# Performance work log

Hardware: AMD Instinct MI355X
Metric: run time of the kernel (lower is better)

The kernel has to match this reference:

```python
import jax, jax.numpy as jnp
import numpy as np
from jax import lax

SIGMA = 1.0
LW = int(4 * SIGMA + 0.5)  # 4 -> 9-tap kernel, matches scipy _gaussian_kernel1d
_xk = np.arange(-LW, LW + 1)
_phi = np.exp(-0.5 * _xk ** 2 / SIGMA ** 2)
GAUSS_K = (_phi / _phi.sum())[::-1].copy()
EPS = 1e-9
HIGH_T, LOW_T = 0.2, 0.1
H = W = 32


def _corr_w(x, k, mode, p):
    # x: (B,H,W); cross-correlate along last dim with 'same' output (torch Conv1d semantics)
    xp = jnp.pad(x, ((0, 0), (0, 0), (p, p)), mode=mode)
    B, Hh, L = xp.shape
    y = lax.conv_general_dilated(xp.reshape(B * Hh, 1, L), k.reshape(1, 1, -1).astype(x.dtype), (1,), 'VALID')
    return y.reshape(B, Hh, L - k.shape[0] + 1)


def _corr_h(x, k, mode, p):
    return jnp.swapaxes(_corr_w(jnp.swapaxes(x, 1, 2), k, mode, p), 1, 2)


def _gauss(x, k):
    # separable gaussian, zero padding (Conv1d padding=lw), both axes
    return _corr_w(_corr_h(x, k, 'constant', LW), k, 'constant', LW)


def _shift(m, di, dj):
    # out[i,j] = m[i+di, j+dj], zeros outside (only interior points are ever selected)
    p = jnp.pad(m, ((0, 0), (1, 1), (1, 1)))
    return p[:, 1 + di:1 + di + H, 1 + dj:1 + dj + W]


def _canny_core(x, mask, with_hyst=True):
    x = x * 0.5 + 0.5
    gray = x[:, 0] * 0.299 + x[:, 1] * 0.587 + x[:, 2] * 0.114  # (B,H,W)
    gk = jnp.asarray(GAUSS_K, gray.dtype)
    bleed = _gauss(mask[:, 0], gk)                      # (1,H,W)
    sm = _gauss(gray, gk) / (bleed + 1e-12)
    s_major = jnp.asarray([-1.0, 0.0, 1.0], sm.dtype)
    s_minor = jnp.asarray([1.0, 2.0, 1.0], sm.dtype)
    # jsobel: derivative along W then smooth along H; isobel: derivative along H then smooth along W
    jsob = _corr_h(_corr_w(sm, s_major, 'edge', 1), s_minor, 'edge', 1)
    isob = _corr_w(_corr_h(sm, s_major, 'edge', 1), s_minor, 'edge', 1)
    ai, aj = jnp.abs(isob), jnp.abs(jsob)
    mag2 = isob ** 2 + jsob ** 2
    mag = jnp.sqrt(mag2 + EPS)
    # binary_erosion of mask with full 3x3 structure, border_value=0
    mb = lax.stop_gradient(mask[0, 0]) != 0
    pm = jnp.pad(mb, 1)
    er2d = jnp.ones((H, W), bool)
    for di in (-1, 0, 1):
        for dj in (-1, 0, 1):
            er2d = er2d & pm[1 + di:1 + di + H, 1 + dj:1 + dj + W]
    # note: torch code builds eroded_mask from batch element 0 only, then reuses for all
    er = (er2d & (lax.stop_gradient(mag2[0]) > 0))[None]  # (1,H,W)
    same = ((isob >= 0) & (jsob >= 0)) | ((isob <= 0) & (jsob <= 0))
    opp = ((isob <= 0) & (jsob >= 0)) | ((isob >= 0) & (jsob <= 0))
    ai_safe = jnp.where(ai > 0, ai, jnp.asarray(1.0, ai.dtype))
    aj_safe = jnp.where(aj > 0, aj, jnp.asarray(1.0, aj.dtype))
    # (selector, w, c1_plus_shift, c2_plus_shift, c1_minus_shift, c2_minus_shift)
    octants = [
        (same & (ai >= aj), aj / (ai + EPS), (1, 0), (1, 1), (-1, 0), (-1, -1)),
        (same & (ai <= aj), ai / aj_safe, (0, 1), (1, 1), (0, -1), (-1, -1)),
        (opp & (ai <= aj), ai / aj_safe, (0, 1), (-1, 1), (0, -1), (1, -1)),
        (opp & (ai >= aj), aj / ai_safe, (-1, 0), (-1, 1), (1, 0), (1, -1)),
    ]
    lm = jnp.zeros(mag.shape, bool)
    for sel, w, p1, p2, m1, m2 in octants:
        pts = er & sel
        ip = _shift(mag, *p2) * w + _shift(mag, *p1) * (1 - w)
        im = _shift(mag, *m2) * w + _shift(mag, *m1) * (1 - w)
        lm = jnp.where(pts, (ip <= mag) & (im <= mag), lm)  # later octants overwrite, like torch
    if not with_hyst:
        return mag, None
    high = lm & (mag >= HIGH_T)
    low = lm & (mag >= LOW_T)

    def dilate(m):
        p = jnp.pad(m, ((0, 0), (1, 1), (1, 1)))
        out = jnp.zeros_like(m)
        for di in (-1, 0, 1):
            for dj in (-1, 0, 1):
                out = out | p[:, 1 + di:1 + di + H, 1 + dj:1 + dj + W]
        return out

    # hysteresis = 8-connected components of `low` that contain a `high` pixel
    def body(c):
        cur, _ = c
        return dilate(cur) & low, cur

    def cond(c):
        cur, prev = c
        return jnp.any(cur != prev)

    final, _ = lax.while_loop(cond, body, (high, jnp.zeros_like(high)))
    return mag, final


def setup_inputs() -> dict:
    key = jax.random.key(0)
    k1, _ = jax.random.split(key)
    x = jax.random.normal(k1, (8192, 3, 32, 32), dtype=jnp.float32)
    mask = jnp.ones((1, 1, 32, 32), dtype=jnp.float32)
    return {"x": x, "mask": mask}


def reference(x, mask):
    mag, final = _canny_core(x, mask, with_hyst=True)
    mf = final.astype(mag.dtype)
    out = mf + mag - lax.stop_gradient(mag)  # straight-through: value==mf, grad flows via mag
    out = (out - 0.5) / 0.5
    return out[:, None]  # (B,1,32,32)
```

## Files before the change

### kernel.cpp

```cpp
#include <hip/hip_runtime.h>
#include <math.h>

#pragma clang fp contract(off)

#define NPIX 1024

__device__ __forceinline__ void compute_gk(float gk[9]) {
    double phi[9];
    #pragma unroll
    for (int t = 0; t < 9; ++t) {
        double d = (double)(t - 4);
        phi[t] = exp(-0.5 * d * d);
    }
    double s = (((phi[0] + phi[1]) + (phi[2] + phi[3])) +
                ((phi[4] + phi[5]) + (phi[6] + phi[7]))) + phi[8];
    #pragma unroll
    for (int t = 0; t < 9; ++t) gk[t] = (float)(phi[t] / s);
}

__device__ __forceinline__ float ldz(const float* b, int i, int j) {
    return (i >= 0 && i < 32 && j >= 0 && j < 32) ? b[(i << 5) + j] : 0.0f;
}
__device__ __forceinline__ float ldc(const float* b, int i, int j) {
    i = i < 0 ? 0 : (i > 31 ? 31 : i);
    j = j < 0 ? 0 : (j > 31 ? 31 : j);
    return b[(i << 5) + j];
}

__device__ __forceinline__ bool nms2(const float* mag, int i, int j, float m, float w,
                                     int p2i, int p2j, int p1i, int p1j,
                                     int m2i, int m2j, int m1i, int m1j) {
    float omw = 1.0f - w;
    float ip = ldz(mag, i + p2i, j + p2j) * w + ldz(mag, i + p1i, j + p1j) * omw;
    float im = ldz(mag, i + m2i, j + m2j) * w + ldz(mag, i + m1i, j + m1j) * omw;
    return (ip <= m) && (im <= m);
}

__global__ __launch_bounds__(256) void canny_pre(const float* __restrict__ x,
                                                 const float* __restrict__ mask,
                                                 float* __restrict__ ws_bleed,
                                                 unsigned int* __restrict__ ws_er,
                                                 float* __restrict__ ws_gk) {
    __shared__ float A[NPIX], Bf[NPIX], C[NPIX], D[NPIX], BL[NPIX];
    __shared__ unsigned int er32[32];
    const int tid = threadIdx.x;
    float gk[9];
    compute_gk(gk);
    if (tid < 9) ws_gk[tid] = gk[tid];

    #pragma unroll
    for (int k = 0; k < 4; ++k) { int p = tid + (k << 8); A[p] = mask[p]; }
    if (tid < 32) er32[tid] = 0u;
    __syncthreads();

    #pragma unroll
    for (int k = 0; k < 4; ++k) {
        int p = tid + (k << 8), i = p >> 5, j = p & 31;
        float s = 0.0f;
        #pragma unroll
        for (int t = 0; t < 9; ++t) s = __fmaf_rn(gk[t], ldz(A, i + t - 4, j), s);
        Bf[p] = s;
    }
    __syncthreads();
    #pragma unroll
    for (int k = 0; k < 4; ++k) {
        int p = tid + (k << 8), i = p >> 5, j = p & 31;
        float s = 0.0f;
        #pragma unroll
        for (int t = 0; t < 9; ++t) s = __fmaf_rn(gk[t], ldz(Bf, i, j + t - 4), s);
        BL[p] = s;
        ws_bleed[p] = s + 1e-12f;
    }

    bool er2d[4];
    #pragma unroll
    for (int k = 0; k < 4; ++k) {
        int p = tid + (k << 8), i = p >> 5, j = p & 31;
        bool e = true;
        for (int di = -1; di <= 1; ++di)
            for (int dj = -1; dj <= 1; ++dj) {
                int ii = i + di, jj = j + dj;
                e = e && (ii >= 0 && ii < 32 && jj >= 0 && jj < 32) && (A[(ii << 5) + jj] != 0.0f);
            }
        er2d[k] = e;
    }
    __syncthreads();

    #pragma unroll
    for (int k = 0; k < 4; ++k) {
        int p = tid + (k << 8);
        float r = x[p]            * 0.5f + 0.5f;
        float g = x[p + NPIX]     * 0.5f + 0.5f;
        float b = x[p + 2 * NPIX] * 0.5f + 0.5f;
        A[p] = r * 0.299f + g * 0.587f + b * 0.114f;
    }
    __syncthreads();
    #pragma unroll
    for (int k = 0; k < 4; ++k) {
        int p = tid + (k << 8), i = p >> 5, j = p & 31;
        float s = 0.0f;
        #pragma unroll
        for (int t = 0; t < 9; ++t) s = __fmaf_rn(gk[t], ldz(A, i + t - 4, j), s);
        Bf[p] = s;
    }
    __syncthreads();
    #pragma unroll
    for (int k = 0; k < 4; ++k) {
        int p = tid + (k << 8), i = p >> 5, j = p & 31;
        float s = 0.0f;
        #pragma unroll
        for (int t = 0; t < 9; ++t) s = __fmaf_rn(gk[t], ldz(Bf, i, j + t - 4), s);
        A[p] = s;
    }
    __syncthreads();
    #pragma unroll
    for (int k = 0; k < 4; ++k) { int p = tid + (k << 8); A[p] = A[p] / (BL[p] + 1e-12f); }
    __syncthreads();
    #pragma unroll
    for (int k = 0; k < 4; ++k) { int p = tid + (k << 8), i = p >> 5, j = p & 31;
        Bf[p] = ldc(A, i, j + 1) - ldc(A, i, j - 1); }
    __syncthreads();
    #pragma unroll
    for (int k = 0; k < 4; ++k) { int p = tid + (k << 8), i = p >> 5, j = p & 31;
        C[p] = (ldc(Bf, i - 1, j) + 2.0f * ldc(Bf, i, j)) + ldc(Bf, i + 1, j); }
    __syncthreads();
    #pragma unroll
    for (int k = 0; k < 4; ++k) { int p = tid + (k << 8), i = p >> 5, j = p & 31;
        Bf[p] = ldc(A, i + 1, j) - ldc(A, i - 1, j); }
    __syncthreads();
    #pragma unroll
    for (int k = 0; k < 4; ++k) { int p = tid + (k << 8), i = p >> 5, j = p & 31;
        D[p] = (ldc(Bf, i, j - 1) + 2.0f * ldc(Bf, i, j)) + ldc(Bf, i, j + 1); }
    __syncthreads();
    #pragma unroll
    for (int k = 0; k < 4; ++k) {
        int p = tid + (k << 8), i = p >> 5, j = p & 31;
        if (er2d[k]) {
            float m2 = D[p] * D[p] + C[p] * C[p];
            if (m2 > 0.0f) atomicOr(&er32[i], 1u << j);
        }
    }
    __syncthreads();
    if (tid < 32) ws_er[tid] = er32[tid];
}

__global__ __launch_bounds__(256) void canny_main(const float* __restrict__ x,
                                                  const float* __restrict__ ws_bleed,
                                                  const unsigned int* __restrict__ ws_er,
                                                  const float* __restrict__ ws_gk,
                                                  float* __restrict__ out) {
    __shared__ float APAD[40 * 32];
    __shared__ float BPAD[32 * 40];
    __shared__ float MPAD[34 * 34];
    __shared__ unsigned int er[32], hi32[32], lo32[32], fin32[32];
    const int tid = threadIdx.x;
    const int b = blockIdx.x;

    float gk[9];
    #pragma unroll
    for (int t = 0; t < 9; ++t) gk[t] = ws_gk[t];

    APAD[tid < 128 ? tid : 1024 + tid] = 0.0f;
    { int r = tid >> 3, c8 = tid & 7; BPAD[r * 40 + c8 + (c8 < 4 ? 0 : 32)] = 0.0f; }
    #pragma unroll
    for (int t = 0; t < 5; ++t) { int idx = tid + (t << 8); if (idx < 34 * 34) MPAD[idx] = 0.0f; }
    if (tid < 32) er[tid] = ws_er[tid];

    {
        const float4* xr = (const float4*)(x + (size_t)b * 3 * NPIX);
        float4 r4 = xr[tid];
        float4 g4 = xr[tid + 256];
        float4 b4 = xr[tid + 512];
        int p = tid << 2, i = p >> 5, j = p & 31;
        float4 gy;
        gy.x = (r4.x * 0.5f + 0.5f) * 0.299f + (g4.x * 0.5f + 0.5f) * 0.587f + (b4.x * 0.5f + 0.5f) * 0.114f;
        gy.y = (r4.y * 0.5f + 0.5f) * 0.299f + (g4.y * 0.5f + 0.5f) * 0.587f + (b4.y * 0.5f + 0.5f) * 0.114f;
        gy.z = (r4.z * 0.5f + 0.5f) * 0.299f + (g4.z * 0.5f + 0.5f) * 0.587f + (b4.z * 0.5f + 0.5f) * 0.114f;
        gy.w = (r4.w * 0.5f + 0.5f) * 0.299f + (g4.w * 0.5f + 0.5f) * 0.587f + (b4.w * 0.5f + 0.5f) * 0.114f;
        *(float4*)&APAD[((i + 4) << 5) + j] = gy;
    }
    __syncthreads();

    #pragma unroll
    for (int k = 0; k < 4; ++k) {
        int p = tid + (k << 8), i = p >> 5, j = p & 31;
        float s = 0.0f;
        #pragma unroll
        for (int t = 0; t < 9; ++t) s = __fmaf_rn(gk[t], APAD[((i + t) << 5) + j], s);
        BPAD[i * 40 + j + 4] = s;
    }
    __syncthreads();

    #pragma unroll
    for (int k = 0; k < 4; ++k) {
        int p = tid + (k << 8), i = p >> 5, j = p & 31;
        float s = 0.0f;
        #pragma unroll
        for (int t = 0; t < 9; ++t) s = __fmaf_rn(gk[t], BPAD[i * 40 + j + t], s);
        APAD[((i + 4) << 5) + j] = s / ws_bleed[p];
    }
    __syncthreads();

    float jsr[4], isr[4], mr[4];
    const float* S = &APAD[4 << 5];
    #pragma unroll
    for (int k = 0; k < 4; ++k) {
        int p = tid + (k << 8), i = p >> 5, j = p & 31;
        int im1 = i > 0 ? i - 1 : 0, ip1 = i < 31 ? i + 1 : 31;
        int jm1 = j > 0 ? j - 1 : 0, jp1 = j < 31 ? j + 1 : 31;
        float tm = S[(im1 << 5) + jp1] - S[(im1 << 5) + jm1];
        float t0 = S[(i   << 5) + jp1] - S[(i   << 5) + jm1];
        float tp = S[(ip1 << 5) + jp1] - S[(ip1 << 5) + jm1];
        float jsob = (tm + 2.0f * t0) + tp;
        float um = S[(ip1 << 5) + jm1] - S[(im1 << 5) + jm1];
        float u0 = S[(ip1 << 5) + j  ] - S[(im1 << 5) + j  ];
        float up = S[(ip1 << 5) + jp1] - S[(im1 << 5) + jp1];
        float isob = (um + 2.0f * u0) + up;
        jsr[k] = jsob; isr[k] = isob;
        float m = sqrtf((isob * isob + jsob * jsob) + 1e-9f);
        mr[k] = m;
        MPAD[(i + 1) * 34 + (j + 1)] = m;
    }
    __syncthreads();

    #pragma unroll
    for (int k = 0; k < 4; ++k) {
        int p = tid + (k << 8), i = p >> 5, j = p & 31;
        float iv = isr[k], jv = jsr[k], m = mr[k];
        float ai = fabsf(iv), aj = fabsf(jv);
        bool same = (iv >= 0.0f && jv >= 0.0f) || (iv <= 0.0f && jv <= 0.0f);
        bool opp  = (iv <= 0.0f && jv >= 0.0f) || (iv >= 0.0f && jv <= 0.0f);
        bool age  = (ai >= aj), ale = (ai <= aj);
        int oct = (opp && age) ? 3 : (opp && ale) ? 2 : (same && ale) ? 1 : 0;
        float ais = ai > 0.0f ? ai : 1.0f;
        float ajs = aj > 0.0f ? aj : 1.0f;
        float num = (oct == 3 || oct == 0) ? aj : ai;
        float den = (oct == 3) ? ais : (oct == 0) ? (ai + 1e-9f) : ajs;
        float w = num / den;
        float omw = 1.0f - w;
        int p2i = (oct >= 2) ? -1 : 1;
        int p1i = (oct == 0) ? 1 : (oct == 3) ? -1 : 0;
        int p1j = (oct == 1 || oct == 2) ? 1 : 0;
        int base = (i + 1) * 34 + (j + 1);
        float ip = MPAD[base + p2i * 34 + 1] * w + MPAD[base + p1i * 34 + p1j] * omw;
        float im = MPAD[base - p2i * 34 - 1] * w + MPAD[base - p1i * 34 - p1j] * omw;
        bool lm = (ip <= m) && (im <= m);
        bool eb = (er[i] >> j) & 1u;
        unsigned long long bh = __ballot(lm && eb && (m >= 0.2f));
        unsigned long long bl = __ballot(lm && eb && (m >= 0.1f));
        if ((tid & 63) == 0) {
            int r0 = (k << 3) + ((tid >> 6) << 1);
            hi32[r0]     = (unsigned int)bh;
            hi32[r0 + 1] = (unsigned int)(bh >> 32);
            lo32[r0]     = (unsigned int)bl;
            lo32[r0 + 1] = (unsigned int)(bl >> 32);
        }
    }
    __syncthreads();

    if (tid < 64) {
        unsigned int lw  = (tid < 32) ? lo32[tid] : 0u;
        unsigned int cur = (tid < 32) ? hi32[tid] : 0u;
        for (;;) {
            unsigned int sp  = cur | (cur << 1) | (cur >> 1);
            unsigned int upv = (unsigned int)__shfl((int)sp, (tid + 63) & 63, 64);
            if (tid == 0) upv = 0u;
            unsigned int dnv = (unsigned int)__shfl((int)sp, (tid + 1) & 63, 64);
            unsigned int nxt = (sp | upv | dnv) & lw;
            bool ch = (nxt != cur);
            cur = nxt;
            if (__ballot((int)ch) == 0ull) break;
        }
        if (tid < 32) fin32[tid] = cur;
    }
    __syncthreads();

    {
        int p = tid << 2, i = p >> 5, j = p & 31;
        unsigned int row = fin32[i];
        float4 o;
        o.x = ((row >> (j    )) & 1u) ? 1.0f : -1.0f;
        o.y = ((row >> (j + 1)) & 1u) ? 1.0f : -1.0f;
        o.z = ((row >> (j + 2)) & 1u) ? 1.0f : -1.0f;
        o.w = ((row >> (j + 3)) & 1u) ? 1.0f : -1.0f;
        ((float4*)(out + (size_t)b * NPIX))[tid] = o;
    }
}

extern "C" void kernel_launch(void* const* d_in, const int* in_sizes, int n_in,
                              void* d_out, int out_size, void* d_ws, size_t ws_size,
                              hipStream_t stream) {
    const float* x    = (const float*)d_in[0];
    const float* mask = (const float*)d_in[1];
    float* out        = (float*)d_out;
    float* ws_bleed   = (float*)d_ws;
    unsigned int* ws_er = (unsigned int*)(ws_bleed + NPIX);
    float* ws_gk      = (float*)(ws_er + 32);
    int Bn = in_sizes[0] / (3 * NPIX);

    hipLaunchKernelGGL(canny_pre, dim3(1), dim3(256), 0, stream, x, mask, ws_bleed, ws_er, ws_gk);
    hipLaunchKernelGGL(canny_main, dim3(Bn), dim3(256), 0, stream, x, ws_bleed, ws_er, ws_gk, out);
}
```

Measured before the change: 51.65 us.

## Process two images per block with interleaved float2 shared-memory layout

Each block now handles two batch images. Their grayscale and blurred values are interleaved as float2 in shared memory, so each LDS access and gaussian tap loop serves both images. Hysteresis runs on a full 64-lane wave with 32 rows per image, with boundaries masked between the two halves. This halves the number of blocks and spreads the per-block overhead (barriers, padding zeroing, loading er/gk) over two images. In exchange it raises shared memory and register use per block, which may reduce occupancy, and the hysteresis loop now runs until the slower of the two images converges.

```diff
diff --git a/kernel.cpp b/kernel.cpp
--- a/kernel.cpp
+++ b/kernel.cpp
@@ -25,15 +25,6 @@
     i = i < 0 ? 0 : (i > 31 ? 31 : i);
     j = j < 0 ? 0 : (j > 31 ? 31 : j);
     return b[(i << 5) + j];
-}
-
-__device__ __forceinline__ bool nms2(const float* mag, int i, int j, float m, float w,
-                                     int p2i, int p2j, int p1i, int p1j,
-                                     int m2i, int m2j, int m1i, int m1j) {
-    float omw = 1.0f - w;
-    float ip = ldz(mag, i + p2i, j + p2j) * w + ldz(mag, i + p1i, j + p1j) * omw;
-    float im = ldz(mag, i + m2i, j + m2j) * w + ldz(mag, i + m1i, j + m1j) * omw;
-    return (ip <= m) && (im <= m);
 }
 
 __global__ __launch_bounds__(256) void canny_pre(const float* __restrict__ x,
@@ -144,49 +135,61 @@
     if (tid < 32) ws_er[tid] = er32[tid];
 }
 
-__global__ __launch_bounds__(256) void canny_main(const float* __restrict__ x,
-                                                  const float* __restrict__ ws_bleed,
-                                                  const unsigned int* __restrict__ ws_er,
-                                                  const float* __restrict__ ws_gk,
-                                                  float* __restrict__ out) {
-    __shared__ float APAD[40 * 32];
-    __shared__ float BPAD[32 * 40];
-    __shared__ float MPAD[34 * 34];
-    __shared__ unsigned int er[32], hi32[32], lo32[32], fin32[32];
+__global__ __launch_bounds__(256) void canny_main2(const float* __restrict__ x,
+                                                   const float* __restrict__ ws_bleed,
+                                                   const unsigned int* __restrict__ ws_er,
+                                                   const float* __restrict__ ws_gk,
+                                                   float* __restrict__ out, int Bn) {
+    __shared__ float2 APAD[40 * 32];
+    __shared__ float2 BPAD[32 * 40];
+    __shared__ float  MP[2][34 * 34];
+    __shared__ unsigned int er[32], hi[64], lo[64], fin[64];
     const int tid = threadIdx.x;
-    const int b = blockIdx.x;
+    const int b0 = blockIdx.x * 2;
+    const int b1 = (b0 + 1 < Bn) ? b0 + 1 : b0;
 
     float gk[9];
     #pragma unroll
     for (int t = 0; t < 9; ++t) gk[t] = ws_gk[t];
 
-    APAD[tid < 128 ? tid : 1024 + tid] = 0.0f;
-    { int r = tid >> 3, c8 = tid & 7; BPAD[r * 40 + c8 + (c8 < 4 ? 0 : 32)] = 0.0f; }
-    #pragma unroll
-    for (int t = 0; t < 5; ++t) { int idx = tid + (t << 8); if (idx < 34 * 34) MPAD[idx] = 0.0f; }
+    const float2 z2 = make_float2(0.0f, 0.0f);
+    APAD[tid < 128 ? tid : 1024 + tid] = z2;
+    { int r = tid >> 3, c8 = tid & 7; BPAD[r * 40 + c8 + (c8 < 4 ? 0 : 32)] = z2; }
+    {
+        float* MZ = &MP[0][0];
+        #pragma unroll
+        for (int t = 0; t < 10; ++t) { int idx = tid + (t << 8); if (idx < 2 * 34 * 34) MZ[idx] = 0.0f; }
+    }
     if (tid < 32) er[tid] = ws_er[tid];
 
     {
-        const float4* xr = (const float4*)(x + (size_t)b * 3 * NPIX);
-        float4 r4 = xr[tid];
-        float4 g4 = xr[tid + 256];
-        float4 b4 = xr[tid + 512];
+        const float4* x0 = (const float4*)(x + (size_t)b0 * 3 * NPIX);
+        const float4* x1 = (const float4*)(x + (size_t)b1 * 3 * NPIX);
+        float4 r0 = x0[tid], g0 = x0[tid + 256], c0 = x0[tid + 512];
+        float4 r1 = x1[tid], g1 = x1[tid + 256], c1 = x1[tid + 512];
         int p = tid << 2, i = p >> 5, j = p & 31;
-        float4 gy;
-        gy.x = (r4.x * 0.5f + 0.5f) * 0.299f + (g4.x * 0.5f + 0.5f) * 0.587f + (b4.x * 0.5f + 0.5f) * 0.114f;
-        gy.y = (r4.y * 0.5f + 0.5f) * 0.299f + (g4.y * 0.5f + 0.5f) * 0.587f + (b4.y * 0.5f + 0.5f) * 0.114f;
-        gy.z = (r4.z * 0.5f + 0.5f) * 0.299f + (g4.z * 0.5f + 0.5f) * 0.587f + (b4.z * 0.5f + 0.5f) * 0.114f;
-        gy.w = (r4.w * 0.5f + 0.5f) * 0.299f + (g4.w * 0.5f + 0.5f) * 0.587f + (b4.w * 0.5f + 0.5f) * 0.114f;
-        *(float4*)&APAD[((i + 4) << 5) + j] = gy;
-    }
-    __syncthreads();
-
-    #pragma unroll
-    for (int k = 0; k < 4; ++k) {
-        int p = tid + (k << 8), i = p >> 5, j = p & 31;
-        float s = 0.0f;
-        #pragma unroll
-        for (int t = 0; t < 9; ++t) s = __fmaf_rn(gk[t], APAD[((i + t) << 5) + j], s);
+        float2* dst = &APAD[((i + 4) << 5) + j];
+        dst[0] = make_float2((r0.x * 0.5f + 0.5f) * 0.299f + (g0.x * 0.5f + 0.5f) * 0.587f + (c0.x * 0.5f + 0.5f) * 0.114f,
+                             (r1.x * 0.5f + 0.5f) * 0.299f + (g1.x * 0.5f + 0.5f) * 0.587f + (c1.x * 0.5f + 0.5f) * 0.114f);
+        dst[1] = make_float2((r0.y * 0.5f + 0.5f) * 0.299f + (g0.y * 0.5f + 0.5f) * 0.587f + (c0.y * 0.5f + 0.5f) * 0.114f,
+                             (r1.y * 0.5f + 0.5f) * 0.299f + (g1.y * 0.5f + 0.5f) * 0.587f + (c1.y * 0.5f + 0.5f) * 0.114f);
+        dst[2] = make_float2((r0.z * 0.5f + 0.5f) * 0.299f + (g0.z * 0.5f + 0.5f) * 0.587f + (c0.z * 0.5f + 0.5f) * 0.114f,
+                             (r1.z * 0.5f + 0.5f) * 0.299f + (g1.z * 0.5f + 0.5f) * 0.587f + (c1.z * 0.5f + 0.5f) * 0.114f);
+        dst[3] = make_float2((r0.w * 0.5f + 0.5f) * 0.299f + (g0.w * 0.5f + 0.5f) * 0.587f + (c0.w * 0.5f + 0.5f) * 0.114f,
+                             (r1.w * 0.5f + 0.5f) * 0.299f + (g1.w * 0.5f + 0.5f) * 0.587f + (c1.w * 0.5f + 0.5f) * 0.114f);
+    }
+    __syncthreads();
+
+    #pragma unroll
+    for (int k = 0; k < 4; ++k) {
+        int p = tid + (k << 8), i = p >> 5, j = p & 31;
+        float2 s = z2;
+        #pragma unroll
+        for (int t = 0; t < 9; ++t) {
+            float2 v = APAD[((i + t) << 5) + j];
+            s.x = __fmaf_rn(gk[t], v.x, s.x);
+            s.y = __fmaf_rn(gk[t], v.y, s.y);
+        }
         BPAD[i * 40 + j + 4] = s;
     }
     __syncthreads();
@@ -194,96 +197,132 @@
     #pragma unroll
     for (int k = 0; k < 4; ++k) {
         int p = tid + (k << 8), i = p >> 5, j = p & 31;
-        float s = 0.0f;
-        #pragma unroll
-        for (int t = 0; t < 9; ++t) s = __fmaf_rn(gk[t], BPAD[i * 40 + j + t], s);
-        APAD[((i + 4) << 5) + j] = s / ws_bleed[p];
-    }
-    __syncthreads();
-
-    float jsr[4], isr[4], mr[4];
-    const float* S = &APAD[4 << 5];
+        float2 s = z2;
+        #pragma unroll
+        for (int t = 0; t < 9; ++t) {
+            float2 v = BPAD[i * 40 + j + t];
+            s.x = __fmaf_rn(gk[t], v.x, s.x);
+            s.y = __fmaf_rn(gk[t], v.y, s.y);
+        }
+        float bl = ws_bleed[p];
+        APAD[((i + 4) << 5) + j] = make_float2(s.x / bl, s.y / bl);
+    }
+    __syncthreads();
+
+    float2 jsr[4], isr[4], mr[4];
+    const float2* S = &APAD[4 << 5];
     #pragma unroll
     for (int k = 0; k < 4; ++k) {
         int p = tid + (k << 8), i = p >> 5, j = p & 31;
         int im1 = i > 0 ? i - 1 : 0, ip1 = i < 31 ? i + 1 : 31;
         int jm1 = j > 0 ? j - 1 : 0, jp1 = j < 31 ? j + 1 : 31;
-        float tm = S[(im1 << 5) + jp1] - S[(im1 << 5) + jm1];
-        float t0 = S[(i   << 5) + jp1] - S[(i   << 5) + jm1];
-        float tp = S[(ip1 << 5) + jp1] - S[(ip1 << 5) + jm1];
-        float jsob = (tm + 2.0f * t0) + tp;
-        float um = S[(ip1 << 5) + jm1] - S[(im1 << 5) + jm1];
-        float u0 = S[(ip1 << 5) + j  ] - S[(im1 << 5) + j  ];
-        float up = S[(ip1 << 5) + jp1] - S[(im1 << 5) + jp1];
-        float isob = (um + 2.0f * u0) + up;
-        jsr[k] = jsob; isr[k] = isob;
-        float m = sqrtf((isob * isob + jsob * jsob) + 1e-9f);
-        mr[k] = m;
-        MPAD[(i + 1) * 34 + (j + 1)] = m;
-    }
-    __syncthreads();
-
-    #pragma unroll
-    for (int k = 0; k < 4; ++k) {
-        int p = tid + (k << 8), i = p >> 5, j = p & 31;
-        float iv = isr[k], jv = jsr[k], m = mr[k];
-        float ai = fabsf(iv), aj = fabsf(jv);
-        bool same = (iv >= 0.0f && jv >= 0.0f) || (iv <= 0.0f && jv <= 0.0f);
-        bool opp  = (iv <= 0.0f && jv >= 0.0f) || (iv >= 0.0f && jv <= 0.0f);
-        bool age  = (ai >= aj), ale = (ai <= aj);
-        int oct = (opp && age) ? 3 : (opp && ale) ? 2 : (same && ale) ? 1 : 0;
-        float ais = ai > 0.0f ? ai : 1.0f;
-        float ajs = aj > 0.0f ? aj : 1.0f;
-        float num = (oct == 3 || oct == 0) ? aj : ai;
-        float den = (oct == 3) ? ais : (oct == 0) ? (ai + 1e-9f) : ajs;
-        float w = num / den;
-        float omw = 1.0f - w;
-        int p2i = (oct >= 2) ? -1 : 1;
-        int p1i = (oct == 0) ? 1 : (oct == 3) ? -1 : 0;
-        int p1j = (oct == 1 || oct == 2) ? 1 : 0;
+        float2 smm = S[(im1 << 5) + jm1], sm0 = S[(im1 << 5) + j], smp = S[(im1 << 5) + jp1];
+        float2 s0m = S[(i   << 5) + jm1],                        s0p = S[(i   << 5) + jp1];
+        float2 spm = S[(ip1 << 5) + jm1], sp0 = S[(ip1 << 5) + j], spp = S[(ip1 << 5) + jp1];
+        float2 jsob, isob, m;
+        {
+            float tm = smp.x - smm.x, t0 = s0p.x - s0m.x, tp = spp.x - spm.x;
+            jsob.x = (tm + 2.0f * t0) + tp;
+            float um = spm.x - smm.x, u0 = sp0.x - sm0.x, up = spp.x - smp.x;
+            isob.x = (um + 2.0f * u0) + up;
+            m.x = sqrtf((isob.x * isob.x + jsob.x * jsob.x) + 1e-9f);
+        }
+        {
+            float tm = smp.y - smm.y, t0 = s0p.y - s0m.y, tp = spp.y - spm.y;
+            jsob.y = (tm + 2.0f * t0) + tp;
+            float um = spm.y - smm.y, u0 = sp0.y - sm0.y, up = spp.y - smp.y;
+            isob.y = (um + 2.0f * u0) + up;
+            m.y = sqrtf((isob.y * isob.y + jsob.y * jsob.y) + 1e-9f);
+        }
+        jsr[k] = jsob; isr[k] = isob; mr[k] = m;
+        int mi = (i + 1) * 34 + (j + 1);
+        MP[0][mi] = m.x;
+        MP[1][mi] = m.y;
+    }
+    __syncthreads();
+
+    #pragma unroll
+    for (int k = 0; k < 4; ++k) {
+        int p = tid + (k << 8), i = p >> 5, j = p & 31;
         int base = (i + 1) * 34 + (j + 1);
-        float ip = MPAD[base + p2i * 34 + 1] * w + MPAD[base + p1i * 34 + p1j] * omw;
-        float im = MPAD[base - p2i * 34 - 1] * w + MPAD[base - p1i * 34 - p1j] * omw;
-        bool lm = (ip <= m) && (im <= m);
         bool eb = (er[i] >> j) & 1u;
-        unsigned long long bh = __ballot(lm && eb && (m >= 0.2f));
-        unsigned long long bl = __ballot(lm && eb && (m >= 0.1f));
+        bool hq[2], lq[2];
+        #pragma unroll
+        for (int c = 0; c < 2; ++c) {
+            float iv = c ? isr[k].y : isr[k].x;
+            float jv = c ? jsr[k].y : jsr[k].x;
+            float m  = c ? mr[k].y  : mr[k].x;
+            float ai = fabsf(iv), aj = fabsf(jv);
+            bool same = (iv >= 0.0f && jv >= 0.0f) || (iv <= 0.0f && jv <= 0.0f);
+            bool opp  = (iv <= 0.0f && jv >= 0.0f) || (iv >= 0.0f && jv <= 0.0f);
+            bool age  = (ai >= aj), ale = (ai <= aj);
+            int oct = (opp && age) ? 3 : (opp && ale) ? 2 : (same && ale) ? 1 : 0;
+            float ais = ai > 0.0f ? ai : 1.0f;
+            float ajs = aj > 0.0f ? aj : 1.0f;
+            float num = (oct == 3 || oct == 0) ? aj : ai;
+            float den = (oct == 3) ? ais : (oct == 0) ? (ai + 1e-9f) : ajs;
+            float w = num / den;
+            float omw = 1.0f - w;
+            int p2i = (oct >= 2) ? -1 : 1;
+            int p1i = (oct == 0) ? 1 : (oct == 3) ? -1 : 0;
+            int p1j = (oct == 1 || oct == 2) ? 1 : 0;
+            const float* MC = MP[c];
+            float ip = MC[base + p2i * 34 + 1] * w + MC[base + p1i * 34 + p1j] * omw;
+            float im = MC[base - p2i * 34 - 1] * w + MC[base - p1i * 34 - p1j] * omw;
+            bool lm = (ip <= m) && (im <= m) && eb;
+            hq[c] = lm && (m >= 0.2f);
+            lq[c] = lm && (m >= 0.1f);
+        }
+        unsigned long long bh0 = __ballot(hq[0]);
+        unsigned long long bl0 = __ballot(lq[0]);
+        unsigned long long bh1 = __ballot(hq[1]);
+        unsigned long long bl1 = __ballot(lq[1]);
         if ((tid & 63) == 0) {
             int r0 = (k << 3) + ((tid >> 6) << 1);
-            hi32[r0]     = (unsigned int)bh;
-            hi32[r0 + 1] = (unsigned int)(bh >> 32);
-            lo32[r0]     = (unsigned int)bl;
-            lo32[r0 + 1] = (unsigned int)(bl >> 32);
+            hi[r0]          = (unsigned int)bh0;
+            hi[r0 + 1]      = (unsigned int)(bh0 >> 32);
+            lo[r0]          = (unsigned int)bl0;
+            lo[r0 + 1]      = (unsigned int)(bl0 >> 32);
+            hi[32 + r0]     = (unsigned int)bh1;
+            hi[32 + r0 + 1] = (unsigned int)(bh1 >> 32);
+            lo[32 + r0]     = (unsigned int)bl1;
+            lo[32 + r0 + 1] = (unsigned int)(bl1 >> 32);
         }
     }
     __syncthreads();
 
     if (tid < 64) {
-        unsigned int lw  = (tid < 32) ? lo32[tid] : 0u;
-        unsigned int cur = (tid < 32) ? hi32[tid] : 0u;
+        unsigned int lw  = lo[tid];
+        unsigned int cur = hi[tid];
         for (;;) {
             unsigned int sp  = cur | (cur << 1) | (cur >> 1);
             unsigned int upv = (unsigned int)__shfl((int)sp, (tid + 63) & 63, 64);
-            if (tid == 0) upv = 0u;
+            if ((tid & 31) == 0) upv = 0u;
             unsigned int dnv = (unsigned int)__shfl((int)sp, (tid + 1) & 63, 64);
+            if ((tid & 31) == 31) dnv = 0u;
             unsigned int nxt = (sp | upv | dnv) & lw;
             bool ch = (nxt != cur);
             cur = nxt;
             if (__ballot((int)ch) == 0ull) break;
         }
-        if (tid < 32) fin32[tid] = cur;
+        fin[tid] = cur;
     }
     __syncthreads();
 
     {
         int p = tid << 2, i = p >> 5, j = p & 31;
-        unsigned int row = fin32[i];
-        float4 o;
-        o.x = ((row >> (j    )) & 1u) ? 1.0f : -1.0f;
-        o.y = ((row >> (j + 1)) & 1u) ? 1.0f : -1.0f;
-        o.z = ((row >> (j + 2)) & 1u) ? 1.0f : -1.0f;
-        o.w = ((row >> (j + 3)) & 1u) ? 1.0f : -1.0f;
-        ((float4*)(out + (size_t)b * NPIX))[tid] = o;
+        unsigned int r0w = fin[i], r1w = fin[32 + i];
+        float4 o0, o1;
+        o0.x = ((r0w >> (j    )) & 1u) ? 1.0f : -1.0f;
+        o0.y = ((r0w >> (j + 1)) & 1u) ? 1.0f : -1.0f;
+        o0.z = ((r0w >> (j + 2)) & 1u) ? 1.0f : -1.0f;
+        o0.w = ((r0w >> (j + 3)) & 1u) ? 1.0f : -1.0f;
+        o1.x = ((r1w >> (j    )) & 1u) ? 1.0f : -1.0f;
+        o1.y = ((r1w >> (j + 1)) & 1u) ? 1.0f : -1.0f;
+        o1.z = ((r1w >> (j + 2)) & 1u) ? 1.0f : -1.0f;
+        o1.w = ((r1w >> (j + 3)) & 1u) ? 1.0f : -1.0f;
+        ((float4*)(out + (size_t)b0 * NPIX))[tid] = o0;
+        if (b1 != b0) ((float4*)(out + (size_t)b1 * NPIX))[tid] = o1;
     }
 }
 
@@ -299,5 +338,6 @@
     int Bn = in_sizes[0] / (3 * NPIX);
 
     hipLaunchKernelGGL(canny_pre, dim3(1), dim3(256), 0, stream, x, mask, ws_bleed, ws_er, ws_gk);
-    hipLaunchKernelGGL(canny_main, dim3(Bn), dim3(256), 0, stream, x, ws_bleed, ws_er, ws_gk, out);
-}
+    hipLaunchKernelGGL(canny_main2, dim3((Bn + 1) / 2), dim3(256), 0, stream,
+                       x, ws_bleed, ws_er, ws_gk, out, Bn);
+}
```

New measurement: 53.77 us. +4.1%, slower.

## Process one image per wavefront to eliminate block-level barriers

Applied to the files above, without the earlier changes.

Restructures the main kernel so each 64-lane wavefront handles a whole image (four images per 256-thread block), with its own LDS slice. All __syncthreads are replaced by compiler memory fences, hysteresis masks stay in registers and move by shuffles, and bleed/erosion values are preloaded into registers. This removes barrier stalls and shared-memory bitmask round trips, at the cost of 16 pixels per lane (more registers and serial work per lane) and reliance on in-wave LDS ordering for correctness.

```diff
diff --git a/kernel.cpp b/kernel.cpp
--- a/kernel.cpp
+++ b/kernel.cpp
@@ -25,15 +25,6 @@
     i = i < 0 ? 0 : (i > 31 ? 31 : i);
     j = j < 0 ? 0 : (j > 31 ? 31 : j);
     return b[(i << 5) + j];
-}
-
-__device__ __forceinline__ bool nms2(const float* mag, int i, int j, float m, float w,
-                                     int p2i, int p2j, int p1i, int p1j,
-                                     int m2i, int m2j, int m1i, int m1j) {
-    float omw = 1.0f - w;
-    float ip = ldz(mag, i + p2i, j + p2j) * w + ldz(mag, i + p1i, j + p1j) * omw;
-    float im = ldz(mag, i + m2i, j + m2j) * w + ldz(mag, i + m1i, j + m1j) * omw;
-    return (ip <= m) && (im <= m);
 }
 
 __global__ __launch_bounds__(256) void canny_pre(const float* __restrict__ x,
@@ -144,88 +135,113 @@
     if (tid < 32) ws_er[tid] = er32[tid];
 }
 
-__global__ __launch_bounds__(256) void canny_main(const float* __restrict__ x,
-                                                  const float* __restrict__ ws_bleed,
-                                                  const unsigned int* __restrict__ ws_er,
-                                                  const float* __restrict__ ws_gk,
-                                                  float* __restrict__ out) {
-    __shared__ float APAD[40 * 32];
-    __shared__ float BPAD[32 * 40];
-    __shared__ float MPAD[34 * 34];
-    __shared__ unsigned int er[32], hi32[32], lo32[32], fin32[32];
+__global__ __launch_bounds__(256) void canny_main4(const float* __restrict__ x,
+                                                   const float* __restrict__ ws_bleed,
+                                                   const unsigned int* __restrict__ ws_er,
+                                                   const float* __restrict__ ws_gk,
+                                                   float* __restrict__ out, int Bn) {
+    __shared__ float lds[4][2560];
     const int tid = threadIdx.x;
-    const int b = blockIdx.x;
+    const int l = tid & 63;
+    const int w = tid >> 6;
+    int b = blockIdx.x * 4 + w;
+    if (b >= Bn) b = Bn - 1;
+    float* A  = lds[w];
+    float* Bq = lds[w] + 1280;
 
     float gk[9];
     #pragma unroll
     for (int t = 0; t < 9; ++t) gk[t] = ws_gk[t];
-
-    APAD[tid < 128 ? tid : 1024 + tid] = 0.0f;
-    { int r = tid >> 3, c8 = tid & 7; BPAD[r * 40 + c8 + (c8 < 4 ? 0 : 32)] = 0.0f; }
-    #pragma unroll
-    for (int t = 0; t < 5; ++t) { int idx = tid + (t << 8); if (idx < 34 * 34) MPAD[idx] = 0.0f; }
-    if (tid < 32) er[tid] = ws_er[tid];
+    unsigned int er_reg = ws_er[l & 31];
+    float blv[16];
+    #pragma unroll
+    for (int k = 0; k < 16; ++k) blv[k] = ws_bleed[l + (k << 6)];
 
     {
+        float4* A4 = (float4*)A;
+        float4* B4 = (float4*)Bq;
+        const float4 z4 = make_float4(0.0f, 0.0f, 0.0f, 0.0f);
+        if (l < 32) A4[l] = z4; else A4[288 + (l - 32)] = z4;
+        { int r = l >> 1, side = l & 1; B4[10 * r + 9 * side] = z4; }
         const float4* xr = (const float4*)(x + (size_t)b * 3 * NPIX);
-        float4 r4 = xr[tid];
-        float4 g4 = xr[tid + 256];
-        float4 b4 = xr[tid + 512];
-        int p = tid << 2, i = p >> 5, j = p & 31;
-        float4 gy;
-        gy.x = (r4.x * 0.5f + 0.5f) * 0.299f + (g4.x * 0.5f + 0.5f) * 0.587f + (b4.x * 0.5f + 0.5f) * 0.114f;
-        gy.y = (r4.y * 0.5f + 0.5f) * 0.299f + (g4.y * 0.5f + 0.5f) * 0.587f + (b4.y * 0.5f + 0.5f) * 0.114f;
-        gy.z = (r4.z * 0.5f + 0.5f) * 0.299f + (g4.z * 0.5f + 0.5f) * 0.587f + (b4.z * 0.5f + 0.5f) * 0.114f;
-        gy.w = (r4.w * 0.5f + 0.5f) * 0.299f + (g4.w * 0.5f + 0.5f) * 0.587f + (b4.w * 0.5f + 0.5f) * 0.114f;
-        *(float4*)&APAD[((i + 4) << 5) + j] = gy;
-    }
-    __syncthreads();
-
-    #pragma unroll
-    for (int k = 0; k < 4; ++k) {
-        int p = tid + (k << 8), i = p >> 5, j = p & 31;
-        float s = 0.0f;
-        #pragma unroll
-        for (int t = 0; t < 9; ++t) s = __fmaf_rn(gk[t], APAD[((i + t) << 5) + j], s);
-        BPAD[i * 40 + j + 4] = s;
-    }
-    __syncthreads();
-
-    #pragma unroll
-    for (int k = 0; k < 4; ++k) {
-        int p = tid + (k << 8), i = p >> 5, j = p & 31;
-        float s = 0.0f;
-        #pragma unroll
-        for (int t = 0; t < 9; ++t) s = __fmaf_rn(gk[t], BPAD[i * 40 + j + t], s);
-        APAD[((i + 4) << 5) + j] = s / ws_bleed[p];
-    }
-    __syncthreads();
-
-    float jsr[4], isr[4], mr[4];
-    const float* S = &APAD[4 << 5];
-    #pragma unroll
-    for (int k = 0; k < 4; ++k) {
-        int p = tid + (k << 8), i = p >> 5, j = p & 31;
-        int im1 = i > 0 ? i - 1 : 0, ip1 = i < 31 ? i + 1 : 31;
-        int jm1 = j > 0 ? j - 1 : 0, jp1 = j < 31 ? j + 1 : 31;
-        float tm = S[(im1 << 5) + jp1] - S[(im1 << 5) + jm1];
-        float t0 = S[(i   << 5) + jp1] - S[(i   << 5) + jm1];
-        float tp = S[(ip1 << 5) + jp1] - S[(ip1 << 5) + jm1];
-        float jsob = (tm + 2.0f * t0) + tp;
-        float um = S[(ip1 << 5) + jm1] - S[(im1 << 5) + jm1];
-        float u0 = S[(ip1 << 5) + j  ] - S[(im1 << 5) + j  ];
-        float up = S[(ip1 << 5) + jp1] - S[(im1 << 5) + jp1];
-        float isob = (um + 2.0f * u0) + up;
-        jsr[k] = jsob; isr[k] = isob;
-        float m = sqrtf((isob * isob + jsob * jsob) + 1e-9f);
-        mr[k] = m;
-        MPAD[(i + 1) * 34 + (j + 1)] = m;
-    }
-    __syncthreads();
-
-    #pragma unroll
-    for (int k = 0; k < 4; ++k) {
-        int p = tid + (k << 8), i = p >> 5, j = p & 31;
+        #pragma unroll
+        for (int k = 0; k < 4; ++k) {
+            int f = l + (k << 6);
+            float4 r4 = xr[f], g4 = xr[f + 256], c4 = xr[f + 512];
+            float4 gy;
+            gy.x = (r4.x * 0.5f + 0.5f) * 0.299f + (g4.x * 0.5f + 0.5f) * 0.587f + (c4.x * 0.5f + 0.5f) * 0.114f;
+            gy.y = (r4.y * 0.5f + 0.5f) * 0.299f + (g4.y * 0.5f + 0.5f) * 0.587f + (c4.y * 0.5f + 0.5f) * 0.114f;
+            gy.z = (r4.z * 0.5f + 0.5f) * 0.299f + (g4.z * 0.5f + 0.5f) * 0.587f + (c4.z * 0.5f + 0.5f) * 0.114f;
+            gy.w = (r4.w * 0.5f + 0.5f) * 0.299f + (g4.w * 0.5f + 0.5f) * 0.587f + (c4.w * 0.5f + 0.5f) * 0.114f;
+            A4[((f >> 3) + 4) * 8 + (f & 7)] = gy;
+        }
+    }
+    asm volatile("" ::: "memory");
+
+    #pragma unroll
+    for (int k = 0; k < 16; ++k) {
+        int p = l + (k << 6), i = p >> 5, j = p & 31;
+        float s = 0.0f;
+        #pragma unroll
+        for (int t = 0; t < 9; ++t) s = __fmaf_rn(gk[t], A[((i + t) << 5) + j], s);
+        Bq[i * 40 + j + 4] = s;
+    }
+    asm volatile("" ::: "memory");
+
+    #pragma unroll
+    for (int k = 0; k < 16; ++k) {
+        int p = l + (k << 6), i = p >> 5, j = p & 31;
+        float s = 0.0f;
+        #pragma unroll
+        for (int t = 0; t < 9; ++t) s = __fmaf_rn(gk[t], Bq[i * 40 + j + t], s);
+        A[((i + 4) << 5) + j] = s / blv[k];
+    }
+    asm volatile("" ::: "memory");
+
+    float jsr[16], isr[16], mr[16];
+    {
+        const float* S = A + 128;
+        #pragma unroll
+        for (int k = 0; k < 16; ++k) {
+            int p = l + (k << 6), i = p >> 5, j = p & 31;
+            int im1 = i > 0 ? i - 1 : 0, ip1 = i < 31 ? i + 1 : 31;
+            int jm1 = j > 0 ? j - 1 : 0, jp1 = j < 31 ? j + 1 : 31;
+            float smm = S[(im1 << 5) + jm1], sm0 = S[(im1 << 5) + j], smp = S[(im1 << 5) + jp1];
+            float s0m = S[(i   << 5) + jm1],                          s0p = S[(i   << 5) + jp1];
+            float spm = S[(ip1 << 5) + jm1], sp0 = S[(ip1 << 5) + j], spp = S[(ip1 << 5) + jp1];
+            float tm = smp - smm, t0 = s0p - s0m, tp = spp - spm;
+            float jsob = (tm + 2.0f * t0) + tp;
+            float um = spm - smm, u0 = sp0 - sm0, up = spp - smp;
+            float isob = (um + 2.0f * u0) + up;
+            jsr[k] = jsob; isr[k] = isob;
+            mr[k] = sqrtf((isob * isob + jsob * jsob) + 1e-9f);
+        }
+    }
+    asm volatile("" ::: "memory");
+
+    #pragma unroll
+    for (int t = 0; t < 3; ++t) {
+        int q = l + (t << 6);
+        if (q < 132) {
+            int idx;
+            if (q < 34)       idx = q;
+            else if (q < 68)  idx = 33 * 34 + (q - 34);
+            else if (q < 100) idx = (q - 67) * 34;
+            else              idx = (q - 99) * 34 + 33;
+            A[idx] = 0.0f;
+        }
+    }
+    #pragma unroll
+    for (int k = 0; k < 16; ++k) {
+        int p = l + (k << 6), i = p >> 5, j = p & 31;
+        A[(i + 1) * 34 + (j + 1)] = mr[k];
+    }
+    asm volatile("" ::: "memory");
+
+    unsigned int myhi = 0u, mylo = 0u;
+    #pragma unroll
+    for (int k = 0; k < 16; ++k) {
+        int p = l + (k << 6), i = p >> 5, j = p & 31;
         float iv = isr[k], jv = jsr[k], m = mr[k];
         float ai = fabsf(iv), aj = fabsf(jv);
         bool same = (iv >= 0.0f && jv >= 0.0f) || (iv <= 0.0f && jv <= 0.0f);
@@ -236,54 +252,55 @@
         float ajs = aj > 0.0f ? aj : 1.0f;
         float num = (oct == 3 || oct == 0) ? aj : ai;
         float den = (oct == 3) ? ais : (oct == 0) ? (ai + 1e-9f) : ajs;
-        float w = num / den;
-        float omw = 1.0f - w;
+        float wq = num / den;
+        float omw = 1.0f - wq;
         int p2i = (oct >= 2) ? -1 : 1;
         int p1i = (oct == 0) ? 1 : (oct == 3) ? -1 : 0;
         int p1j = (oct == 1 || oct == 2) ? 1 : 0;
         int base = (i + 1) * 34 + (j + 1);
-        float ip = MPAD[base + p2i * 34 + 1] * w + MPAD[base + p1i * 34 + p1j] * omw;
-        float im = MPAD[base - p2i * 34 - 1] * w + MPAD[base - p1i * 34 - p1j] * omw;
+        float ip = A[base + p2i * 34 + 1] * wq + A[base + p1i * 34 + p1j] * omw;
+        float im = A[base - p2i * 34 - 1] * wq + A[base - p1i * 34 - p1j] * omw;
         bool lm = (ip <= m) && (im <= m);
-        bool eb = (er[i] >> j) & 1u;
+        unsigned int ew = (unsigned int)__shfl((int)er_reg, (k << 1) + (l >> 5), 64);
+        bool eb = (ew >> (l & 31)) & 1u;
         unsigned long long bh = __ballot(lm && eb && (m >= 0.2f));
         unsigned long long bl = __ballot(lm && eb && (m >= 0.1f));
-        if ((tid & 63) == 0) {
-            int r0 = (k << 3) + ((tid >> 6) << 1);
-            hi32[r0]     = (unsigned int)bh;
-            hi32[r0 + 1] = (unsigned int)(bh >> 32);
-            lo32[r0]     = (unsigned int)bl;
-            lo32[r0 + 1] = (unsigned int)(bl >> 32);
-        }
-    }
-    __syncthreads();
-
-    if (tid < 64) {
-        unsigned int lw  = (tid < 32) ? lo32[tid] : 0u;
-        unsigned int cur = (tid < 32) ? hi32[tid] : 0u;
+        if (l < 32 && (l >> 1) == k) {
+            myhi = (l & 1) ? (unsigned int)(bh >> 32) : (unsigned int)bh;
+            mylo = (l & 1) ? (unsigned int)(bl >> 32) : (unsigned int)bl;
+        }
+    }
+
+    unsigned int cur = myhi;
+    {
+        const unsigned int lw = mylo;
         for (;;) {
             unsigned int sp  = cur | (cur << 1) | (cur >> 1);
-            unsigned int upv = (unsigned int)__shfl((int)sp, (tid + 63) & 63, 64);
-            if (tid == 0) upv = 0u;
-            unsigned int dnv = (unsigned int)__shfl((int)sp, (tid + 1) & 63, 64);
-            unsigned int nxt = (sp | upv | dnv) & lw;
+            unsigned int up  = (unsigned int)__shfl((int)sp, (l + 63) & 63, 64);
+            if ((l & 31) == 0) up = 0u;
+            unsigned int dn  = (unsigned int)__shfl((int)sp, (l + 1) & 63, 64);
+            if ((l & 31) == 31) dn = 0u;
+            unsigned int nxt = (sp | up | dn) & lw;
             bool ch = (nxt != cur);
             cur = nxt;
             if (__ballot((int)ch) == 0ull) break;
         }
-        if (tid < 32) fin32[tid] = cur;
-    }
-    __syncthreads();
+    }
 
     {
-        int p = tid << 2, i = p >> 5, j = p & 31;
-        unsigned int row = fin32[i];
-        float4 o;
-        o.x = ((row >> (j    )) & 1u) ? 1.0f : -1.0f;
-        o.y = ((row >> (j + 1)) & 1u) ? 1.0f : -1.0f;
-        o.z = ((row >> (j + 2)) & 1u) ? 1.0f : -1.0f;
-        o.w = ((row >> (j + 3)) & 1u) ? 1.0f : -1.0f;
-        ((float4*)(out + (size_t)b * NPIX))[tid] = o;
+        float4* o4 = (float4*)(out + (size_t)b * NPIX);
+        #pragma unroll
+        for (int k = 0; k < 4; ++k) {
+            int f = l + (k << 6);
+            unsigned int wd = (unsigned int)__shfl((int)cur, f >> 3, 64);
+            int j0 = (f & 7) << 2;
+            float4 o;
+            o.x = ((wd >> (j0    )) & 1u) ? 1.0f : -1.0f;
+            o.y = ((wd >> (j0 + 1)) & 1u) ? 1.0f : -1.0f;
+            o.z = ((wd >> (j0 + 2)) & 1u) ? 1.0f : -1.0f;
+            o.w = ((wd >> (j0 + 3)) & 1u) ? 1.0f : -1.0f;
+            o4[f] = o;
+        }
     }
 }
 
@@ -299,5 +316,6 @@
     int Bn = in_sizes[0] / (3 * NPIX);
 
     hipLaunchKernelGGL(canny_pre, dim3(1), dim3(256), 0, stream, x, mask, ws_bleed, ws_er, ws_gk);
-    hipLaunchKernelGGL(canny_main, dim3(Bn), dim3(256), 0, stream, x, ws_bleed, ws_er, ws_gk, out);
-}
+    hipLaunchKernelGGL(canny_main4, dim3((Bn + 3) / 4), dim3(256), 0, stream,
+                       x, ws_bleed, ws_er, ws_gk, out, Bn);
+}
```

Result: slower. 60.89 us (+17.9%).

## Process four contiguous pixels per thread with float4 LDS loads and register windows

Applied to the files above, without the earlier changes.

Switches the main kernel from one pixel per thread with a 256-pixel stride to four horizontally adjacent pixels per thread. The vertical blur, horizontal blur and Sobel stages use float4 shared-memory loads and sliding register windows, which cuts the number of LDS reads and the redundant neighbour loads. Hysteresis row masks are built from per-thread bitmasks combined with shfl_xor instead of wave ballots. The cost is higher register pressure and the extra clamp handling at row edges.

```diff
diff --git a/kernel.cpp b/kernel.cpp
--- a/kernel.cpp
+++ b/kernel.cpp
@@ -25,15 +25,6 @@
     i = i < 0 ? 0 : (i > 31 ? 31 : i);
     j = j < 0 ? 0 : (j > 31 ? 31 : j);
     return b[(i << 5) + j];
-}
-
-__device__ __forceinline__ bool nms2(const float* mag, int i, int j, float m, float w,
-                                     int p2i, int p2j, int p1i, int p1j,
-                                     int m2i, int m2j, int m1i, int m1j) {
-    float omw = 1.0f - w;
-    float ip = ldz(mag, i + p2i, j + p2j) * w + ldz(mag, i + p1i, j + p1j) * omw;
-    float im = ldz(mag, i + m2i, j + m2j) * w + ldz(mag, i + m1i, j + m1j) * omw;
-    return (ip <= m) && (im <= m);
 }
 
 __global__ __launch_bounds__(256) void canny_pre(const float* __restrict__ x,
@@ -155,6 +146,8 @@
     __shared__ unsigned int er[32], hi32[32], lo32[32], fin32[32];
     const int tid = threadIdx.x;
     const int b = blockIdx.x;
+    const int i  = tid >> 3;
+    const int j0 = (tid & 7) << 2;
 
     float gk[9];
     #pragma unroll
@@ -168,93 +161,137 @@
 
     {
         const float4* xr = (const float4*)(x + (size_t)b * 3 * NPIX);
-        float4 r4 = xr[tid];
-        float4 g4 = xr[tid + 256];
-        float4 b4 = xr[tid + 512];
-        int p = tid << 2, i = p >> 5, j = p & 31;
+        float4 r4 = xr[tid], g4 = xr[tid + 256], c4 = xr[tid + 512];
         float4 gy;
-        gy.x = (r4.x * 0.5f + 0.5f) * 0.299f + (g4.x * 0.5f + 0.5f) * 0.587f + (b4.x * 0.5f + 0.5f) * 0.114f;
-        gy.y = (r4.y * 0.5f + 0.5f) * 0.299f + (g4.y * 0.5f + 0.5f) * 0.587f + (b4.y * 0.5f + 0.5f) * 0.114f;
-        gy.z = (r4.z * 0.5f + 0.5f) * 0.299f + (g4.z * 0.5f + 0.5f) * 0.587f + (b4.z * 0.5f + 0.5f) * 0.114f;
-        gy.w = (r4.w * 0.5f + 0.5f) * 0.299f + (g4.w * 0.5f + 0.5f) * 0.587f + (b4.w * 0.5f + 0.5f) * 0.114f;
-        *(float4*)&APAD[((i + 4) << 5) + j] = gy;
-    }
-    __syncthreads();
-
-    #pragma unroll
-    for (int k = 0; k < 4; ++k) {
-        int p = tid + (k << 8), i = p >> 5, j = p & 31;
-        float s = 0.0f;
-        #pragma unroll
-        for (int t = 0; t < 9; ++t) s = __fmaf_rn(gk[t], APAD[((i + t) << 5) + j], s);
-        BPAD[i * 40 + j + 4] = s;
-    }
-    __syncthreads();
-
-    #pragma unroll
-    for (int k = 0; k < 4; ++k) {
-        int p = tid + (k << 8), i = p >> 5, j = p & 31;
-        float s = 0.0f;
-        #pragma unroll
-        for (int t = 0; t < 9; ++t) s = __fmaf_rn(gk[t], BPAD[i * 40 + j + t], s);
-        APAD[((i + 4) << 5) + j] = s / ws_bleed[p];
+        gy.x = (r4.x * 0.5f + 0.5f) * 0.299f + (g4.x * 0.5f + 0.5f) * 0.587f + (c4.x * 0.5f + 0.5f) * 0.114f;
+        gy.y = (r4.y * 0.5f + 0.5f) * 0.299f + (g4.y * 0.5f + 0.5f) * 0.587f + (c4.y * 0.5f + 0.5f) * 0.114f;
+        gy.z = (r4.z * 0.5f + 0.5f) * 0.299f + (g4.z * 0.5f + 0.5f) * 0.587f + (c4.z * 0.5f + 0.5f) * 0.114f;
+        gy.w = (r4.w * 0.5f + 0.5f) * 0.299f + (g4.w * 0.5f + 0.5f) * 0.587f + (c4.w * 0.5f + 0.5f) * 0.114f;
+        *(float4*)&APAD[((i + 4) << 5) + j0] = gy;
+    }
+    __syncthreads();
+
+    {
+        float4 acc = make_float4(0.0f, 0.0f, 0.0f, 0.0f);
+        #pragma unroll
+        for (int t = 0; t < 9; ++t) {
+            float4 v = *(const float4*)&APAD[((i + t) << 5) + j0];
+            acc.x = __fmaf_rn(gk[t], v.x, acc.x);
+            acc.y = __fmaf_rn(gk[t], v.y, acc.y);
+            acc.z = __fmaf_rn(gk[t], v.z, acc.z);
+            acc.w = __fmaf_rn(gk[t], v.w, acc.w);
+        }
+        *(float4*)&BPAD[i * 40 + j0 + 4] = acc;
+    }
+    __syncthreads();
+
+    {
+        const float* bp = &BPAD[i * 40 + j0];
+        float4 w0 = *(const float4*)bp;
+        float4 w1 = *(const float4*)(bp + 4);
+        float4 w2 = *(const float4*)(bp + 8);
+        float win[12] = {w0.x, w0.y, w0.z, w0.w, w1.x, w1.y, w1.z, w1.w,
+                         w2.x, w2.y, w2.z, w2.w};
+        float4 bl4 = *(const float4*)(ws_bleed + (tid << 2));
+        float4 sm4;
+        float s;
+        s = 0.0f;
+        #pragma unroll
+        for (int t = 0; t < 9; ++t) s = __fmaf_rn(gk[t], win[0 + t], s);
+        sm4.x = s / bl4.x;
+        s = 0.0f;
+        #pragma unroll
+        for (int t = 0; t < 9; ++t) s = __fmaf_rn(gk[t], win[1 + t], s);
+        sm4.y = s / bl4.y;
+        s = 0.0f;
+        #pragma unroll
+        for (int t = 0; t < 9; ++t) s = __fmaf_rn(gk[t], win[2 + t], s);
+        sm4.z = s / bl4.z;
+        s = 0.0f;
+        #pragma unroll
+        for (int t = 0; t < 9; ++t) s = __fmaf_rn(gk[t], win[3 + t], s);
+        sm4.w = s / bl4.w;
+        *(float4*)&APAD[((i + 4) << 5) + j0] = sm4;
     }
     __syncthreads();
 
     float jsr[4], isr[4], mr[4];
-    const float* S = &APAD[4 << 5];
-    #pragma unroll
-    for (int k = 0; k < 4; ++k) {
-        int p = tid + (k << 8), i = p >> 5, j = p & 31;
-        int im1 = i > 0 ? i - 1 : 0, ip1 = i < 31 ? i + 1 : 31;
-        int jm1 = j > 0 ? j - 1 : 0, jp1 = j < 31 ? j + 1 : 31;
-        float tm = S[(im1 << 5) + jp1] - S[(im1 << 5) + jm1];
-        float t0 = S[(i   << 5) + jp1] - S[(i   << 5) + jm1];
-        float tp = S[(ip1 << 5) + jp1] - S[(ip1 << 5) + jm1];
-        float jsob = (tm + 2.0f * t0) + tp;
-        float um = S[(ip1 << 5) + jm1] - S[(im1 << 5) + jm1];
-        float u0 = S[(ip1 << 5) + j  ] - S[(im1 << 5) + j  ];
-        float up = S[(ip1 << 5) + jp1] - S[(im1 << 5) + jp1];
-        float isob = (um + 2.0f * u0) + up;
-        jsr[k] = jsob; isr[k] = isob;
-        float m = sqrtf((isob * isob + jsob * jsob) + 1e-9f);
-        mr[k] = m;
-        MPAD[(i + 1) * 34 + (j + 1)] = m;
-    }
-    __syncthreads();
-
-    #pragma unroll
-    for (int k = 0; k < 4; ++k) {
-        int p = tid + (k << 8), i = p >> 5, j = p & 31;
-        float iv = isr[k], jv = jsr[k], m = mr[k];
-        float ai = fabsf(iv), aj = fabsf(jv);
-        bool same = (iv >= 0.0f && jv >= 0.0f) || (iv <= 0.0f && jv <= 0.0f);
-        bool opp  = (iv <= 0.0f && jv >= 0.0f) || (iv >= 0.0f && jv <= 0.0f);
-        bool age  = (ai >= aj), ale = (ai <= aj);
-        int oct = (opp && age) ? 3 : (opp && ale) ? 2 : (same && ale) ? 1 : 0;
-        float ais = ai > 0.0f ? ai : 1.0f;
-        float ajs = aj > 0.0f ? aj : 1.0f;
-        float num = (oct == 3 || oct == 0) ? aj : ai;
-        float den = (oct == 3) ? ais : (oct == 0) ? (ai + 1e-9f) : ajs;
-        float w = num / den;
-        float omw = 1.0f - w;
-        int p2i = (oct >= 2) ? -1 : 1;
-        int p1i = (oct == 0) ? 1 : (oct == 3) ? -1 : 0;
-        int p1j = (oct == 1 || oct == 2) ? 1 : 0;
-        int base = (i + 1) * 34 + (j + 1);
-        float ip = MPAD[base + p2i * 34 + 1] * w + MPAD[base + p1i * 34 + p1j] * omw;
-        float im = MPAD[base - p2i * 34 - 1] * w + MPAD[base - p1i * 34 - p1j] * omw;
-        bool lm = (ip <= m) && (im <= m);
-        bool eb = (er[i] >> j) & 1u;
-        unsigned long long bh = __ballot(lm && eb && (m >= 0.2f));
-        unsigned long long bl = __ballot(lm && eb && (m >= 0.1f));
-        if ((tid & 63) == 0) {
-            int r0 = (k << 3) + ((tid >> 6) << 1);
-            hi32[r0]     = (unsigned int)bh;
-            hi32[r0 + 1] = (unsigned int)(bh >> 32);
-            lo32[r0]     = (unsigned int)bl;
-            lo32[r0 + 1] = (unsigned int)(bl >> 32);
-        }
+    {
+        const float* S = APAD + 128;
+        const int im1 = i > 0 ? i - 1 : 0, ip1 = i < 31 ? i + 1 : 31;
+        const bool le = (j0 == 0), re = (j0 == 28);
+        float am[6], a0[6], ap[6];
+        {
+            const float* r = S + (im1 << 5) + j0 - 4;
+            float4 v0 = *(const float4*)r, v1 = *(const float4*)(r + 4), v2 = *(const float4*)(r + 8);
+            am[0] = le ? v1.x : v0.w; am[1] = v1.x; am[2] = v1.y; am[3] = v1.z; am[4] = v1.w;
+            am[5] = re ? v1.w : v2.x;
+        }
+        {
+            const float* r = S + (i << 5) + j0 - 4;
+            float4 v0 = *(const float4*)r, v1 = *(const float4*)(r + 4), v2 = *(const float4*)(r + 8);
+            a0[0] = le ? v1.x : v0.w; a0[1] = v1.x; a0[2] = v1.y; a0[3] = v1.z; a0[4] = v1.w;
+            a0[5] = re ? v1.w : v2.x;
+        }
+        {
+            const float* r = S + (ip1 << 5) + j0 - 4;
+            float4 v0 = *(const float4*)r, v1 = *(const float4*)(r + 4), v2 = *(const float4*)(r + 8);
+            ap[0] = le ? v1.x : v0.w; ap[1] = v1.x; ap[2] = v1.y; ap[3] = v1.z; ap[4] = v1.w;
+            ap[5] = re ? v1.w : v2.x;
+        }
+        #pragma unroll
+        for (int q = 0; q < 4; ++q) {
+            float tm = am[q + 2] - am[q];
+            float t0 = a0[q + 2] - a0[q];
+            float tp = ap[q + 2] - ap[q];
+            float jsob = (tm + 2.0f * t0) + tp;
+            float um = ap[q] - am[q];
+            float u0 = ap[q + 1] - am[q + 1];
+            float up = ap[q + 2] - am[q + 2];
+            float isob = (um + 2.0f * u0) + up;
+            jsr[q] = jsob; isr[q] = isob;
+            float m = sqrtf((isob * isob + jsob * jsob) + 1e-9f);
+            mr[q] = m;
+            MPAD[(i + 1) * 34 + (j0 + q + 1)] = m;
+        }
+    }
+    __syncthreads();
+
+    {
+        unsigned int ew = er[i];
+        unsigned int hn = 0u, ln = 0u;
+        #pragma unroll
+        for (int q = 0; q < 4; ++q) {
+            int j = j0 + q;
+            float iv = isr[q], jv = jsr[q], m = mr[q];
+            float ai = fabsf(iv), aj = fabsf(jv);
+            bool same = (iv >= 0.0f && jv >= 0.0f) || (iv <= 0.0f && jv <= 0.0f);
+            bool opp  = (iv <= 0.0f && jv >= 0.0f) || (iv >= 0.0f && jv <= 0.0f);
+            bool age  = (ai >= aj), ale = (ai <= aj);
+            int oct = (opp && age) ? 3 : (opp && ale) ? 2 : (same && ale) ? 1 : 0;
+            float ais = ai > 0.0f ? ai : 1.0f;
+            float ajs = aj > 0.0f ? aj : 1.0f;
+            float num = (oct == 3 || oct == 0) ? aj : ai;
+            float den = (oct == 3) ? ais : (oct == 0) ? (ai + 1e-9f) : ajs;
+            float wq = num / den;
+            float omw = 1.0f - wq;
+            int p2i = (oct >= 2) ? -1 : 1;
+            int p1i = (oct == 0) ? 1 : (oct == 3) ? -1 : 0;
+            int p1j = (oct == 1 || oct == 2) ? 1 : 0;
+            int base = (i + 1) * 34 + (j + 1);
+            float ipv = MPAD[base + p2i * 34 + 1] * wq + MPAD[base + p1i * 34 + p1j] * omw;
+            float imv = MPAD[base - p2i * 34 - 1] * wq + MPAD[base - p1i * 34 - p1j] * omw;
+            bool lm = (ipv <= m) && (imv <= m);
+            bool eb = (ew >> j) & 1u;
+            if (lm && eb && (m >= 0.2f)) hn |= (1u << j);
+            if (lm && eb && (m >= 0.1f)) ln |= (1u << j);
+        }
+        #pragma unroll
+        for (int mset = 1; mset < 8; mset <<= 1) {
+            hn |= (unsigned int)__shfl_xor((int)hn, mset, 64);
+            ln |= (unsigned int)__shfl_xor((int)ln, mset, 64);
+        }
+        if ((tid & 7) == 0) { hi32[i] = hn; lo32[i] = ln; }
     }
     __syncthreads();
 
@@ -276,13 +313,12 @@
     __syncthreads();
 
     {
-        int p = tid << 2, i = p >> 5, j = p & 31;
         unsigned int row = fin32[i];
         float4 o;
-        o.x = ((row >> (j    )) & 1u) ? 1.0f : -1.0f;
-        o.y = ((row >> (j + 1)) & 1u) ? 1.0f : -1.0f;
-        o.z = ((row >> (j + 2)) & 1u) ? 1.0f : -1.0f;
-        o.w = ((row >> (j + 3)) & 1u) ? 1.0f : -1.0f;
+        o.x = ((row >> (j0    )) & 1u) ? 1.0f : -1.0f;
+        o.y = ((row >> (j0 + 1)) & 1u) ? 1.0f : -1.0f;
+        o.z = ((row >> (j0 + 2)) & 1u) ? 1.0f : -1.0f;
+        o.w = ((row >> (j0 + 3)) & 1u) ? 1.0f : -1.0f;
         ((float4*)(out + (size_t)b * NPIX))[tid] = o;
     }
 }
```

After: 52.71 us. 1.02x slower.
